# Optimization experiments

Measured on AMD Instinct MI355X. Metric: run time of the kernel, lower is better.

The kernel has to match this reference:

```python
import jax, jax.numpy as jnp
import numpy as np

N_NODES = 100000
N_EDGES = 1600000
IN_DIM, EDGE_DIM, HID, HEADS = 2, 1, 64, 4
NEG_SLOPE = 0.2


def setup_inputs() -> dict:
    key = jax.random.key(0)
    ks = jax.random.split(key, 20)
    p = lambda k, shape: (jax.random.normal(k, shape, dtype=jnp.float32) * 0.1)
    inp = {
        "x": jax.random.normal(ks[0], (N_NODES, IN_DIM), dtype=jnp.float32),
        "edge_index": jax.random.randint(ks[1], (2, N_EDGES), 0, N_NODES, dtype=jnp.int32),
        "edge_attr": jax.random.uniform(ks[2], (N_EDGES, EDGE_DIM), dtype=jnp.float32),
        # conv1: heads=4, out=64, concat=True
        "W1": p(ks[3], (IN_DIM, HEADS * HID)),
        "We1": p(ks[4], (EDGE_DIM, HEADS * HID)),
        "as1": p(ks[5], (HEADS, HID)),
        "ad1": p(ks[6], (HEADS, HID)),
        "ae1": p(ks[7], (HEADS, HID)),
        "b1": jnp.zeros((HEADS * HID,), jnp.float32),
        # conv2: heads=1, out=64
        "W2": p(ks[8], (HEADS * HID, HID)),
        "We2": p(ks[9], (EDGE_DIM, HID)),
        "as2": p(ks[10], (1, HID)),
        "ad2": p(ks[11], (1, HID)),
        "ae2": p(ks[12], (1, HID)),
        "b2": jnp.zeros((HID,), jnp.float32),
        "Wr1": p(ks[13], (HID, HID)),
        "br1": jnp.zeros((HID,), jnp.float32),
        "Wr2": p(ks[14], (HID, 1)),
        "br2": jnp.zeros((1,), jnp.float32),
    }
    return inp


def gat_layer(x, src, dst, edge_attr, W, We, a_src, a_dst, a_edge, bias, heads, out_dim, n_nodes):
    """PyG GATConv (add_self_loops=False, concat=True, edge_dim set)."""
    h = (x @ W).reshape(n_nodes, heads, out_dim)          # [N,H,D]
    he = (edge_attr @ We).reshape(-1, heads, out_dim)     # [E,H,D]
    al_s = jnp.sum(h * a_src, axis=-1)                    # [N,H]
    al_d = jnp.sum(h * a_dst, axis=-1)                    # [N,H]
    al_e = jnp.sum(he * a_edge, axis=-1)                  # [E,H]
    logits = jax.nn.leaky_relu(al_s[src] + al_d[dst] + al_e, NEG_SLOPE)  # [E,H]
    # segment softmax over destination node
    m = jax.ops.segment_max(logits, dst, num_segments=n_nodes)
    p = jnp.exp(logits - m[dst])
    z = jax.ops.segment_sum(p, dst, num_segments=n_nodes)
    alpha = p / (z[dst] + 1e-16)                          # [E,H]
    msg = alpha[:, :, None] * h[src]                      # [E,H,D]
    out = jax.ops.segment_sum(msg, dst, num_segments=n_nodes)
    return out.reshape(n_nodes, heads * out_dim) + bias


def reference(x, edge_index, edge_attr, W1, We1, as1, ad1, ae1, b1,
              W2, We2, as2, ad2, ae2, b2, Wr1, br1, Wr2, br2):
    src, dst = edge_index[0], edge_index[1]
    n = x.shape[0]
    h = gat_layer(x, src, dst, edge_attr, W1, We1, as1, ad1, ae1, b1, HEADS, HID, n)
    h = gat_layer(h, src, dst, edge_attr, W2, We2, as2, ad2, ae2, b2, 1, HID, n)
    edge_emb = h[src] + h[dst]                             # [E,HID]
    hidden = jax.nn.relu(edge_emb @ Wr1 + br1)
    return (hidden @ Wr2 + br2).squeeze(-1)                # [E]
```

## Files before the change

### kernel.cpp

```cpp
#include <hip/hip_runtime.h>
#include <hip/hip_bf16.h>
#include <hip/hip_fp16.h>

#define NEG_SLOPE 0.2f
#define NBUCK_MAX 256
#define BCAP 12288
#define TILE 2048

__device__ __forceinline__ float lrelu(float v) { return v >= 0.f ? v : NEG_SLOPE * v; }

__device__ __forceinline__ float wave_sum(float v) {
    for (int o = 32; o; o >>= 1) v += __shfl_down(v, o, 64);
    return v;
}

__device__ __forceinline__ void h8_to_f(const uint4 v, float* f) {
    float2 a = __half22float2(*(const __half2*)&v.x);
    float2 b = __half22float2(*(const __half2*)&v.y);
    float2 c = __half22float2(*(const __half2*)&v.z);
    float2 d = __half22float2(*(const __half2*)&v.w);
    f[0] = a.x; f[1] = a.y; f[2] = b.x; f[3] = b.y;
    f[4] = c.x; f[5] = c.y; f[6] = d.x; f[7] = d.y;
}

__device__ __forceinline__ void compute_ce1(const float* __restrict__ We1,
                                            const float* __restrict__ ae1,
                                            float* ce ) {
    int t = threadIdx.x;
    float p = wave_sum(We1[t] * ae1[t]);
    if ((t & 63) == 0) ce[t >> 6] = p;
    __syncthreads();
}

__device__ __forceinline__ float compute_ce2(const float* __restrict__ We2,
                                             const float* __restrict__ ae2,
                                             float* sh ) {
    int t = threadIdx.x;
    if (t < 64) {
        float p = wave_sum(We2[t] * ae2[t]);
        if (t == 0) sh[0] = p;
    }
    __syncthreads();
    return sh[0];
}

__global__ __launch_bounds__(256) void prep1_kernel(
    const float* __restrict__ x, const float* __restrict__ W1,
    const float* __restrict__ as1, const float* __restrict__ ad1,
    const float* __restrict__ W2, const float* __restrict__ b1,
    const float* __restrict__ Wr1, const float* __restrict__ b2,
    const float* __restrict__ as2, const float* __restrict__ ad2,
    float* __restrict__ al_s1, float* __restrict__ al_d1,
    int* __restrict__ bucket_cur, float* __restrict__ V, int N) {
    __shared__ float cs0[4], cs1[4], cd0[4], cd1[4];
    __shared__ float sV0[256], sV1[256], sc[64];
    int t = threadIdx.x;
    if (blockIdx.x == 0) bucket_cur[t] = t * BCAP;
    {
        float a = as1[t], d = ad1[t], u0 = W1[t], u1 = W1[256 + t];
        float p0 = wave_sum(u0 * a);
        float p1 = wave_sum(u1 * a);
        float q0 = wave_sum(u0 * d);
        float q1 = wave_sum(u1 * d);
        if ((t & 63) == 0) {
            int h = t >> 6;
            cs0[h] = p0; cs1[h] = p1; cd0[h] = q0; cd1[h] = q1;
        }
    }
    __syncthreads();
    int n = blockIdx.x * 256 + t;
    if (n < N) {
        float2 xs = ((const float2*)x)[n];
        float4 vs, vd;
        vs.x = xs.x * cs0[0] + xs.y * cs1[0];
        vs.y = xs.x * cs0[1] + xs.y * cs1[1];
        vs.z = xs.x * cs0[2] + xs.y * cs1[2];
        vs.w = xs.x * cs0[3] + xs.y * cs1[3];
        vd.x = xs.x * cd0[0] + xs.y * cd1[0];
        vd.y = xs.x * cd0[1] + xs.y * cd1[1];
        vd.z = xs.x * cd0[2] + xs.y * cd1[2];
        vd.w = xs.x * cd0[3] + xs.y * cd1[3];
        ((float4*)al_s1)[n] = vs;
        ((float4*)al_d1)[n] = vd;
    }
    if (blockIdx.x == 0) {
        int h = t >> 6, j = t & 63;
        float v0 = 0.f, v1 = 0.f;
        for (int k = 0; k < 64; ++k) {
            float w2 = W2[(h * 64 + k) * 64 + j];
            v0 += W1[h * 64 + k] * w2;
            v1 += W1[256 + h * 64 + k] * w2;
        }
        sV0[t] = v0;
        sV1[t] = v1;
        if (t < 64) {
            float c = 0.f;
            for (int i = 0; i < 256; ++i) c += b1[i] * W2[i * 64 + t];
            sc[t] = c;
        }
        __syncthreads();
        float v0w = 0.f, v1w = 0.f;
        for (int k = 0; k < 64; ++k) {
            float wr = Wr1[k * 64 + j];
            v0w += sV0[h * 64 + k] * wr;
            v1w += sV1[h * 64 + k] * wr;
        }
        V[t] = v0w;
        V[256 + t] = v1w;
        if (t < 64) {
            float cw = 0.f, cb = 0.f;
            for (int k = 0; k < 64; ++k) {
                float wr = Wr1[k * 64 + t];
                cw += sc[k] * wr;
                cb += b2[k] * wr;
            }
            V[512 + t] = cw;
            V[576 + t] = cb;
        }
        int lane = t & 63;
        float p0 = wave_sum(sV0[t] * as2[lane]);
        float p1 = wave_sum(sV1[t] * as2[lane]);
        float q0 = wave_sum(sV0[t] * ad2[lane]);
        float q1 = wave_sum(sV1[t] * ad2[lane]);
        if (lane == 0) {
            V[640 + h] = p0; V[644 + h] = p1; V[648 + h] = q0; V[652 + h] = q1;
        }
        if (t < 64) {
            float r0 = wave_sum(sc[t] * as2[t]);
            float r1 = wave_sum(sc[t] * ad2[t]);
            if (t == 0) { V[656] = r0; V[657] = r1; }
        }
    }
}

__global__ __launch_bounds__(256) void binA_kernel(
    const int* __restrict__ ei, const float* __restrict__ ea,
    int* __restrict__ bucket_cur, uint2* __restrict__ ebm, int E, int nbuck) {
    __shared__ int cnt[NBUCK_MAX];
    __shared__ int gbase[NBUCK_MAX];
    __shared__ int lofs[NBUCK_MAX];
    __shared__ int psum[NBUCK_MAX];
    __shared__ uint2 buf[TILE];
    __shared__ unsigned short bkt[TILE];
    int t = threadIdx.x;
    int e0 = blockIdx.x * TILE;
    int cntE = min(TILE, E - e0);
    for (int i = t; i < nbuck; i += 256) cnt[i] = 0;
    __syncthreads();
    uint2 rec[8];
    int rb[8], rr[8];
#pragma unroll
    for (int i = 0; i < 8; ++i) {
        int e = e0 + i * 256 + t;
        if (i * 256 + t < cntE) {
            int s = ei[e], d = ei[E + e];
            unsigned q = (unsigned)(ea[e] * 32767.f + 0.5f);
            q = min(q, 32767u);
            rec[i] = make_uint2((((unsigned)s) << 15) | q,
                                (unsigned)(((d & 511) << 21) | e));
            rb[i] = d >> 9;
            rr[i] = atomicAdd(&cnt[rb[i]], 1);
        } else {
            rb[i] = -1;
        }
    }
    __syncthreads();
    int v = (t < nbuck) ? cnt[t] : 0;
    psum[t] = v;
    __syncthreads();
    for (int o = 1; o < 256; o <<= 1) {
        int a = (t >= o) ? psum[t - o] : 0;
        __syncthreads();
        psum[t] += a;
        __syncthreads();
    }
    if (t < nbuck) {
        lofs[t] = psum[t] - v;
        if (v) gbase[t] = atomicAdd(&bucket_cur[t], v);
    }
    __syncthreads();
#pragma unroll
    for (int i = 0; i < 8; ++i) {
        if (rb[i] >= 0) {
            int p = lofs[rb[i]] + rr[i];
            buf[p] = rec[i];
            bkt[p] = (unsigned short)rb[i];
        }
    }
    __syncthreads();
    for (int p = t; p < cntE; p += 256) {
        int b = bkt[p];
        ebm[gbase[b] + (p - lofs[b])] = buf[p];
    }
}

__global__ __launch_bounds__(256) void binB_kernel(
    const uint2* __restrict__ ebm, const int* __restrict__ bucket_cur,
    int* __restrict__ deg, int* __restrict__ offs,
    unsigned* __restrict__ csr_se, int N) {
    __shared__ int lcnt[512];
    __shared__ int lofs[512];
    __shared__ int lcur[512];
    int b = blockIdx.x;
    int n0 = b << 9;
    int t = threadIdx.x;
    lcnt[t] = 0; lcnt[t + 256] = 0;
    __syncthreads();
    int bstart = b * BCAP;
    int bend = bucket_cur[b];
    for (int p = bstart + t; p < bend; p += 256)
        atomicAdd(&lcnt[ebm[p].y >> 21], 1);
    __syncthreads();
    int a0 = lcnt[2 * t], a1 = lcnt[2 * t + 1];
    __shared__ int psum[256];
    psum[t] = a0 + a1;
    __syncthreads();
    for (int o = 1; o < 256; o <<= 1) {
        int a = (t >= o) ? psum[t - o] : 0;
        __syncthreads();
        psum[t] += a;
        __syncthreads();
    }
    int excl = psum[t] - (a0 + a1);
    lofs[2 * t] = excl;
    lofs[2 * t + 1] = excl + a0;
    lcur[2 * t] = bstart + excl;
    lcur[2 * t + 1] = bstart + excl + a0;
    __syncthreads();
    for (int i = t; i < 512; i += 256) {
        int n = n0 + i;
        if (n < N) {
            deg[n] = lcnt[i];
            offs[n] = bstart + lofs[i] + lcnt[i];
        }
    }
    for (int p = bstart + t; p < bend; p += 256) {
        uint2 m = ebm[p];
        int pos = atomicAdd(&lcur[m.y >> 21], 1);
        csr_se[pos] = m.x;
    }
}

__global__ __launch_bounds__(256) void aggX_kernel(
    const unsigned* __restrict__ csr_se, const int* __restrict__ offs,
    const int* __restrict__ deg,
    const float* __restrict__ al_s1, const float* __restrict__ al_d1,
    const float* __restrict__ x,
    const float* __restrict__ We1, const float* __restrict__ ae1,
    const float* __restrict__ V,
    float2* __restrict__ XA, float* __restrict__ al_s2, float* __restrict__ al_d2,
    int N) {
    __shared__ float ce[4];
    __shared__ float sS[18];
    if (threadIdx.x < 18) sS[threadIdx.x] = V[640 + threadIdx.x];
    compute_ce1(We1, ae1, ce);
    int t = blockIdx.x * 256 + threadIdx.x;
    int n = t >> 2, h = t & 3;
    if (n >= N) return;
    int dc = deg[n];
    int start = offs[n] - dc;
    float ald = al_d1[4 * n + h];
    float ceh = ce[h] * (1.f / 32767.f);
    const float2* x2 = (const float2*)x;
    float z = 0.f, X0 = 0.f, X1 = 0.f;
    int j = 0;
    for (; j + 2 <= dc; j += 2) {
        unsigned w0 = csr_se[start + j];
        unsigned w1 = csr_se[start + j + 1];
        int s0 = w0 >> 15, s1 = w1 >> 15;
        float als0 = al_s1[4 * s0 + h];
        float als1 = al_s1[4 * s1 + h];
        float2 xs0 = x2[s0];
        float2 xs1 = x2[s1];
        float e0 = __expf(lrelu(als0 + ald + (float)(w0 & 32767u) * ceh));
        float e1 = __expf(lrelu(als1 + ald + (float)(w1 & 32767u) * ceh));
        z += e0 + e1;
        X0 += e0 * xs0.x + e1 * xs1.x;
        X1 += e0 * xs0.y + e1 * xs1.y;
    }
    if (j < dc) {
        unsigned w = csr_se[start + j];
        int s = w >> 15;
        float als = al_s1[4 * s + h];
        float2 xs = x2[s];
        float ex = __expf(lrelu(als + ald + (float)(w & 32767u) * ceh));
        z += ex;
        X0 += ex * xs.x;
        X1 += ex * xs.y;
    }
    float inv = 1.f / (z + 1e-16f);
    float xa0 = X0 * inv, xa1 = X1 * inv;
    XA[(size_t)4 * n + h] = make_float2(xa0, xa1);
    float ps = xa0 * sS[h] + xa1 * sS[4 + h];
    float pd = xa0 * sS[8 + h] + xa1 * sS[12 + h];
    ps += __shfl_xor(ps, 1, 64); ps += __shfl_xor(ps, 2, 64);
    pd += __shfl_xor(pd, 1, 64); pd += __shfl_xor(pd, 2, 64);
    if (h == 0) {
        al_s2[n] = sS[16] + ps;
        al_d2[n] = sS[17] + pd;
    }
}

__global__ __launch_bounds__(256) void msg2y_kernel(
    const unsigned* __restrict__ csr_se, const int* __restrict__ offs,
    const int* __restrict__ deg,
    const float* __restrict__ al_s2, const float* __restrict__ al_d2,
    const float* __restrict__ We2, const float* __restrict__ ae2,
    const float2* __restrict__ XA,
    uint4* __restrict__ Yh, float* __restrict__ w0n, int N) {
    __shared__ float sh[1];
    float ce2 = compute_ce2(We2, ae2, sh) * (1.f / 32767.f);
    int t = blockIdx.x * 256 + threadIdx.x;
    int n = t >> 2, q = t & 3;
    if (n >= N) return;
    int dc = deg[n];
    int start = offs[n] - dc;
    float ald = al_d2[n];
    const float4* xa4 = (const float4*)XA;
    float y0 = 0.f, y1 = 0.f, y2 = 0.f, y3 = 0.f;
    float y4 = 0.f, y5 = 0.f, y6 = 0.f, y7 = 0.f;
    float z = 0.f;
    int j = q;
    for (; j + 4 < dc; j += 8) {
        unsigned wA = csr_se[start + j];
        unsigned wB = csr_se[start + j + 4];
        int sA = wA >> 15, sB = wB >> 15;
        float alsA = al_s2[sA];
        float alsB = al_s2[sB];
        float4 a0 = xa4[(size_t)sA * 2];
        float4 a1 = xa4[(size_t)sA * 2 + 1];
        float4 b0 = xa4[(size_t)sB * 2];
        float4 b1 = xa4[(size_t)sB * 2 + 1];
        float exA = __expf(lrelu(alsA + ald + (float)(wA & 32767u) * ce2));
        float exB = __expf(lrelu(alsB + ald + (float)(wB & 32767u) * ce2));
        z += exA + exB;
        y0 += exA * a0.x + exB * b0.x;
        y1 += exA * a0.y + exB * b0.y;
        y2 += exA * a0.z + exB * b0.z;
        y3 += exA * a0.w + exB * b0.w;
        y4 += exA * a1.x + exB * b1.x;
        y5 += exA * a1.y + exB * b1.y;
        y6 += exA * a1.z + exB * b1.z;
        y7 += exA * a1.w + exB * b1.w;
    }
    if (j < dc) {
        unsigned w = csr_se[start + j];
        int s = w >> 15;
        float als = al_s2[s];
        float4 a0 = xa4[(size_t)s * 2];
        float4 a1 = xa4[(size_t)s * 2 + 1];
        float ex = __expf(lrelu(als + ald + (float)(w & 32767u) * ce2));
        z += ex;
        y0 += ex * a0.x; y1 += ex * a0.y; y2 += ex * a0.z; y3 += ex * a0.w;
        y4 += ex * a1.x; y5 += ex * a1.y; y6 += ex * a1.z; y7 += ex * a1.w;
    }
    y0 += __shfl_xor(y0, 1, 64); y0 += __shfl_xor(y0, 2, 64);
    y1 += __shfl_xor(y1, 1, 64); y1 += __shfl_xor(y1, 2, 64);
    y2 += __shfl_xor(y2, 1, 64); y2 += __shfl_xor(y2, 2, 64);
    y3 += __shfl_xor(y3, 1, 64); y3 += __shfl_xor(y3, 2, 64);
    y4 += __shfl_xor(y4, 1, 64); y4 += __shfl_xor(y4, 2, 64);
    y5 += __shfl_xor(y5, 1, 64); y5 += __shfl_xor(y5, 2, 64);
    y6 += __shfl_xor(y6, 1, 64); y6 += __shfl_xor(y6, 2, 64);
    y7 += __shfl_xor(y7, 1, 64); y7 += __shfl_xor(y7, 2, 64);
    z += __shfl_xor(z, 1, 64); z += __shfl_xor(z, 2, 64);
    if (q == 0) {
        float inv = 1.f / (z + 1e-16f);
        __half2 p0 = __floats2half2_rn(y0 * inv, y1 * inv);
        __half2 p1 = __floats2half2_rn(y2 * inv, y3 * inv);
        __half2 p2 = __floats2half2_rn(y4 * inv, y5 * inv);
        __half2 p3 = __floats2half2_rn(y6 * inv, y7 * inv);
        uint4 o;
        o.x = *(unsigned*)&p0; o.y = *(unsigned*)&p1;
        o.z = *(unsigned*)&p2; o.w = *(unsigned*)&p3;
        Yh[n] = o;
        w0n[n] = z * inv;
    }
}

__global__ __launch_bounds__(256) void edge_kernel(
    const int* __restrict__ ei,
    const uint4* __restrict__ Yh, const float* __restrict__ w0n,
    const float* __restrict__ V,
    const float* __restrict__ br1, const float* __restrict__ Wr2,
    const float* __restrict__ br2, float* __restrict__ out, int E) {
    int e = blockIdx.x * 256 + threadIdx.x;
    if (e >= E) return;
    int s = ei[e], d = ei[E + e];
    uint4 ys = Yh[s], yd = Yh[d];
    float w0 = w0n[s] + w0n[d];
    float fs[8], fd[8], tt[8];
    h8_to_f(ys, fs);
    h8_to_f(yd, fd);
#pragma unroll
    for (int i = 0; i < 8; ++i) tt[i] = fs[i] + fd[i];
    float acc = 0.f;
#pragma unroll
    for (int k = 0; k < 64; ++k) {
        float g = fmaf(w0, V[512 + k], fmaf(2.f, V[576 + k], br1[k]));
        g = fmaf(tt[0], V[k],       g);
        g = fmaf(tt[1], V[256 + k], g);
        g = fmaf(tt[2], V[64 + k],  g);
        g = fmaf(tt[3], V[320 + k], g);
        g = fmaf(tt[4], V[128 + k], g);
        g = fmaf(tt[5], V[384 + k], g);
        g = fmaf(tt[6], V[192 + k], g);
        g = fmaf(tt[7], V[448 + k], g);
        acc = fmaf(fmaxf(g, 0.f), Wr2[k], acc);
    }
    out[e] = acc + br2[0];
}

extern "C" void kernel_launch(void* const* d_in, const int* in_sizes, int n_in,
                              void* d_out, int out_size, void* d_ws, size_t ws_size,
                              hipStream_t stream) {
    const float* x    = (const float*)d_in[0];
    const int*   ei   = (const int*)d_in[1];
    const float* ea   = (const float*)d_in[2];
    const float* W1   = (const float*)d_in[3];
    const float* We1  = (const float*)d_in[4];
    const float* as1  = (const float*)d_in[5];
    const float* ad1  = (const float*)d_in[6];
    const float* ae1  = (const float*)d_in[7];
    const float* b1   = (const float*)d_in[8];
    const float* W2   = (const float*)d_in[9];
    const float* We2  = (const float*)d_in[10];
    const float* as2  = (const float*)d_in[11];
    const float* ad2  = (const float*)d_in[12];
    const float* ae2  = (const float*)d_in[13];
    const float* b2   = (const float*)d_in[14];
    const float* Wr1  = (const float*)d_in[15];
    const float* br1  = (const float*)d_in[16];
    const float* Wr2  = (const float*)d_in[17];
    const float* br2  = (const float*)d_in[18];
    float* out = (float*)d_out;

    const int N = in_sizes[0] / 2;
    const int E = in_sizes[2];
    const int nbuck = (N + 511) >> 9;
    const size_t capE = (size_t)nbuck * BCAP;

    float* ws = (float*)d_ws;
    float*    al_s1 = ws;
    float*    al_d1 = al_s1 + (size_t)N * 4;
    float*    al_s2 = al_d1 + (size_t)N * 4;
    float*    al_d2 = al_s2 + N;
    float2*   XA    = (float2*)((((uintptr_t)(al_d2 + N)) + 31) & ~(uintptr_t)31);
    float*    V     = (float*)((((uintptr_t)(XA + (size_t)N * 4)) + 15) & ~(uintptr_t)15);
    int*      deg   = (int*)(V + 704);
    int*      offs  = deg + N;
    int*      bucket_cur  = offs + N;
    uint4*    Yh    = (uint4*)((((uintptr_t)(bucket_cur + 256)) + 15) & ~(uintptr_t)15);
    float*    w0n   = (float*)(Yh + N);
    uint2*    ebm   = (uint2*)((((uintptr_t)(w0n + N)) + 15) & ~(uintptr_t)15);
    unsigned* csr_se = (unsigned*)(ebm + capE);

    const int nb = (N + 255) / 256;

    prep1_kernel<<<nb, 256, 0, stream>>>(x, W1, as1, ad1, W2, b1, Wr1, b2, as2, ad2,
                                         al_s1, al_d1, bucket_cur, V, N);
    binA_kernel<<<(E + TILE - 1) / TILE, 256, 0, stream>>>(ei, ea, bucket_cur, ebm,
                                                           E, nbuck);
    binB_kernel<<<nbuck, 256, 0, stream>>>(ebm, bucket_cur, deg, offs, csr_se, N);
    aggX_kernel<<<(4 * N + 255) / 256, 256, 0, stream>>>(csr_se, offs, deg,
                                                         al_s1, al_d1, x, We1, ae1, V,
                                                         XA, al_s2, al_d2, N);
    msg2y_kernel<<<(4 * N + 255) / 256, 256, 0, stream>>>(csr_se, offs, deg,
                                                          al_s2, al_d2, We2, ae2, XA,
                                                          Yh, w0n, N);
    edge_kernel<<<(E + 255) / 256, 256, 0, stream>>>(ei, Yh, w0n, V, br1, Wr2, br2,
                                                     out, E);
}
```

Baseline: 241.8 us.

## Pack per-node gather records, recompute layer-2 source logits, vectorize edge MLP

Layer-1 source logits and node features are packed into one 32-byte record per node, so each neighbour gather in aggX reads a single cache line instead of two separate arrays. msg2y now recomputes the layer-2 source attention logit from the XA values it already loads, which removes a separate random gather of al_s2. The edge MLP folds the constant bias terms into one precomputed vector and processes two hidden units per iteration with packed float2 arithmetic to cut instruction count. The costs are extra FMAs per neighbour in msg2y and a larger record array in the workspace.

```diff
diff --git a/kernel.cpp b/kernel.cpp
--- a/kernel.cpp
+++ b/kernel.cpp
@@ -6,6 +6,8 @@
 #define NBUCK_MAX 256
 #define BCAP 12288
 #define TILE 2048
+
+typedef float v2f __attribute__((ext_vector_type(2)));
 
 __device__ __forceinline__ float lrelu(float v) { return v >= 0.f ? v : NEG_SLOPE * v; }
 
@@ -50,7 +52,8 @@
     const float* __restrict__ W2, const float* __restrict__ b1,
     const float* __restrict__ Wr1, const float* __restrict__ b2,
     const float* __restrict__ as2, const float* __restrict__ ad2,
-    float* __restrict__ al_s1, float* __restrict__ al_d1,
+    const float* __restrict__ br1,
+    float* __restrict__ rec, float* __restrict__ al_d1,
     int* __restrict__ bucket_cur, float* __restrict__ V, int N) {
     __shared__ float cs0[4], cs1[4], cd0[4], cd1[4];
     __shared__ float sV0[256], sV1[256], sc[64];
@@ -80,7 +83,8 @@
         vd.y = xs.x * cd0[1] + xs.y * cd1[1];
         vd.z = xs.x * cd0[2] + xs.y * cd1[2];
         vd.w = xs.x * cd0[3] + xs.y * cd1[3];
-        ((float4*)al_s1)[n] = vs;
+        ((float4*)rec)[2 * n] = vs;
+        ((float4*)rec)[2 * n + 1] = make_float4(xs.x, xs.y, 0.f, 0.f);
         ((float4*)al_d1)[n] = vd;
     }
     if (blockIdx.x == 0) {
@@ -116,6 +120,7 @@
             }
             V[512 + t] = cw;
             V[576 + t] = cb;
+            V[672 + t] = 2.f * cb + br1[t];
         }
         int lane = t & 63;
         float p0 = wave_sum(sV0[t] * as2[lane]);
@@ -244,8 +249,7 @@
 __global__ __launch_bounds__(256) void aggX_kernel(
     const unsigned* __restrict__ csr_se, const int* __restrict__ offs,
     const int* __restrict__ deg,
-    const float* __restrict__ al_s1, const float* __restrict__ al_d1,
-    const float* __restrict__ x,
+    const float* __restrict__ rec, const float* __restrict__ al_d1,
     const float* __restrict__ We1, const float* __restrict__ ae1,
     const float* __restrict__ V,
     float2* __restrict__ XA, float* __restrict__ al_s2, float* __restrict__ al_d2,
@@ -261,17 +265,18 @@
     int start = offs[n] - dc;
     float ald = al_d1[4 * n + h];
     float ceh = ce[h] * (1.f / 32767.f);
-    const float2* x2 = (const float2*)x;
     float z = 0.f, X0 = 0.f, X1 = 0.f;
     int j = 0;
     for (; j + 2 <= dc; j += 2) {
         unsigned w0 = csr_se[start + j];
         unsigned w1 = csr_se[start + j + 1];
         int s0 = w0 >> 15, s1 = w1 >> 15;
-        float als0 = al_s1[4 * s0 + h];
-        float als1 = al_s1[4 * s1 + h];
-        float2 xs0 = x2[s0];
-        float2 xs1 = x2[s1];
+        const float* rb0 = rec + (size_t)8 * s0;
+        const float* rb1 = rec + (size_t)8 * s1;
+        float als0 = rb0[h];
+        float als1 = rb1[h];
+        float2 xs0 = *(const float2*)(rb0 + 4);
+        float2 xs1 = *(const float2*)(rb1 + 4);
         float e0 = __expf(lrelu(als0 + ald + (float)(w0 & 32767u) * ceh));
         float e1 = __expf(lrelu(als1 + ald + (float)(w1 & 32767u) * ceh));
         z += e0 + e1;
@@ -281,8 +286,9 @@
     if (j < dc) {
         unsigned w = csr_se[start + j];
         int s = w >> 15;
-        float als = al_s1[4 * s + h];
-        float2 xs = x2[s];
+        const float* rb = rec + (size_t)8 * s;
+        float als = rb[h];
+        float2 xs = *(const float2*)(rb + 4);
         float ex = __expf(lrelu(als + ald + (float)(w & 32767u) * ceh));
         z += ex;
         X0 += ex * xs.x;
@@ -304,12 +310,16 @@
 __global__ __launch_bounds__(256) void msg2y_kernel(
     const unsigned* __restrict__ csr_se, const int* __restrict__ offs,
     const int* __restrict__ deg,
-    const float* __restrict__ al_s2, const float* __restrict__ al_d2,
+    const float* __restrict__ al_d2,
     const float* __restrict__ We2, const float* __restrict__ ae2,
+    const float* __restrict__ V,
     const float2* __restrict__ XA,
     uint4* __restrict__ Yh, float* __restrict__ w0n, int N) {
     __shared__ float sh[1];
     float ce2 = compute_ce2(We2, ae2, sh) * (1.f / 32767.f);
+    float s16 = V[656];
+    float ss0 = V[640], ss1 = V[641], ss2 = V[642], ss3 = V[643];
+    float ss4 = V[644], ss5 = V[645], ss6 = V[646], ss7 = V[647];
     int t = blockIdx.x * 256 + threadIdx.x;
     int n = t >> 2, q = t & 3;
     if (n >= N) return;
@@ -325,12 +335,14 @@
         unsigned wA = csr_se[start + j];
         unsigned wB = csr_se[start + j + 4];
         int sA = wA >> 15, sB = wB >> 15;
-        float alsA = al_s2[sA];
-        float alsB = al_s2[sB];
         float4 a0 = xa4[(size_t)sA * 2];
         float4 a1 = xa4[(size_t)sA * 2 + 1];
         float4 b0 = xa4[(size_t)sB * 2];
         float4 b1 = xa4[(size_t)sB * 2 + 1];
+        float alsA = s16 + a0.x * ss0 + a0.y * ss4 + a0.z * ss1 + a0.w * ss5
+                         + a1.x * ss2 + a1.y * ss6 + a1.z * ss3 + a1.w * ss7;
+        float alsB = s16 + b0.x * ss0 + b0.y * ss4 + b0.z * ss1 + b0.w * ss5
+                         + b1.x * ss2 + b1.y * ss6 + b1.z * ss3 + b1.w * ss7;
         float exA = __expf(lrelu(alsA + ald + (float)(wA & 32767u) * ce2));
         float exB = __expf(lrelu(alsB + ald + (float)(wB & 32767u) * ce2));
         z += exA + exB;
@@ -346,9 +358,10 @@
     if (j < dc) {
         unsigned w = csr_se[start + j];
         int s = w >> 15;
-        float als = al_s2[s];
         float4 a0 = xa4[(size_t)s * 2];
         float4 a1 = xa4[(size_t)s * 2 + 1];
+        float als = s16 + a0.x * ss0 + a0.y * ss4 + a0.z * ss1 + a0.w * ss5
+                        + a1.x * ss2 + a1.y * ss6 + a1.z * ss3 + a1.w * ss7;
         float ex = __expf(lrelu(als + ald + (float)(w & 32767u) * ce2));
         z += ex;
         y0 += ex * a0.x; y1 += ex * a0.y; y2 += ex * a0.z; y3 += ex * a0.w;
@@ -381,7 +394,7 @@
     const int* __restrict__ ei,
     const uint4* __restrict__ Yh, const float* __restrict__ w0n,
     const float* __restrict__ V,
-    const float* __restrict__ br1, const float* __restrict__ Wr2,
+    const float* __restrict__ Wr2,
     const float* __restrict__ br2, float* __restrict__ out, int E) {
     int e = blockIdx.x * 256 + threadIdx.x;
     if (e >= E) return;
@@ -393,21 +406,24 @@
     h8_to_f(yd, fd);
 #pragma unroll
     for (int i = 0; i < 8; ++i) tt[i] = fs[i] + fd[i];
-    float acc = 0.f;
+    v2f acc = {0.f, 0.f};
+    v2f w0v = {w0, w0};
 #pragma unroll
-    for (int k = 0; k < 64; ++k) {
-        float g = fmaf(w0, V[512 + k], fmaf(2.f, V[576 + k], br1[k]));
-        g = fmaf(tt[0], V[k],       g);
-        g = fmaf(tt[1], V[256 + k], g);
-        g = fmaf(tt[2], V[64 + k],  g);
-        g = fmaf(tt[3], V[320 + k], g);
-        g = fmaf(tt[4], V[128 + k], g);
-        g = fmaf(tt[5], V[384 + k], g);
-        g = fmaf(tt[6], V[192 + k], g);
-        g = fmaf(tt[7], V[448 + k], g);
-        acc = fmaf(fmaxf(g, 0.f), Wr2[k], acc);
-    }
-    out[e] = acc + br2[0];
+    for (int k = 0; k < 64; k += 2) {
+        v2f g = w0v * (*(const v2f*)(V + 512 + k));
+        g += *(const v2f*)(V + 672 + k);
+        g += (v2f){tt[0], tt[0]} * (*(const v2f*)(V + k));
+        g += (v2f){tt[1], tt[1]} * (*(const v2f*)(V + 256 + k));
+        g += (v2f){tt[2], tt[2]} * (*(const v2f*)(V + 64 + k));
+        g += (v2f){tt[3], tt[3]} * (*(const v2f*)(V + 320 + k));
+        g += (v2f){tt[4], tt[4]} * (*(const v2f*)(V + 128 + k));
+        g += (v2f){tt[5], tt[5]} * (*(const v2f*)(V + 384 + k));
+        g += (v2f){tt[6], tt[6]} * (*(const v2f*)(V + 192 + k));
+        g += (v2f){tt[7], tt[7]} * (*(const v2f*)(V + 448 + k));
+        g = __builtin_elementwise_max(g, (v2f){0.f, 0.f});
+        acc += g * (*(const v2f*)(Wr2 + k));
+    }
+    out[e] = acc.x + acc.y + br2[0];
 }
 
 extern "C" void kernel_launch(void* const* d_in, const int* in_sizes, int n_in,
@@ -440,13 +456,13 @@
     const size_t capE = (size_t)nbuck * BCAP;
 
     float* ws = (float*)d_ws;
-    float*    al_s1 = ws;
-    float*    al_d1 = al_s1 + (size_t)N * 4;
+    float*    rec   = ws;
+    float*    al_d1 = rec + (size_t)N * 8;
     float*    al_s2 = al_d1 + (size_t)N * 4;
     float*    al_d2 = al_s2 + N;
     float2*   XA    = (float2*)((((uintptr_t)(al_d2 + N)) + 31) & ~(uintptr_t)31);
     float*    V     = (float*)((((uintptr_t)(XA + (size_t)N * 4)) + 15) & ~(uintptr_t)15);
-    int*      deg   = (int*)(V + 704);
+    int*      deg   = (int*)(V + 768);
     int*      offs  = deg + N;
     int*      bucket_cur  = offs + N;
     uint4*    Yh    = (uint4*)((((uintptr_t)(bucket_cur + 256)) + 15) & ~(uintptr_t)15);
@@ -457,16 +473,16 @@
     const int nb = (N + 255) / 256;
 
     prep1_kernel<<<nb, 256, 0, stream>>>(x, W1, as1, ad1, W2, b1, Wr1, b2, as2, ad2,
-                                         al_s1, al_d1, bucket_cur, V, N);
+                                         br1, rec, al_d1, bucket_cur, V, N);
     binA_kernel<<<(E + TILE - 1) / TILE, 256, 0, stream>>>(ei, ea, bucket_cur, ebm,
                                                            E, nbuck);
     binB_kernel<<<nbuck, 256, 0, stream>>>(ebm, bucket_cur, deg, offs, csr_se, N);
     aggX_kernel<<<(4 * N + 255) / 256, 256, 0, stream>>>(csr_se, offs, deg,
-                                                         al_s1, al_d1, x, We1, ae1, V,
+                                                         rec, al_d1, We1, ae1, V,
                                                          XA, al_s2, al_d2, N);
     msg2y_kernel<<<(4 * N + 255) / 256, 256, 0, stream>>>(csr_se, offs, deg,
-                                                          al_s2, al_d2, We2, ae2, XA,
+                                                          al_d2, We2, ae2, V, XA,
                                                           Yh, w0n, N);
-    edge_kernel<<<(E + 255) / 256, 256, 0, stream>>>(ei, Yh, w0n, V, br1, Wr2, br2,
+    edge_kernel<<<(E + 255) / 256, 256, 0, stream>>>(ei, Yh, w0n, V, Wr2, br2,
                                                      out, E);
 }
```

New measurement: 223.2 us (median of 2 runs). 1.08x faster.
